# Performance work log

Measured on AMD Instinct MI355X. Metric: run time of the kernel, lower is better.

Reference implementation:

```python
import jax, jax.numpy as jnp
import numpy as np

N_HEAD = 4
GROUPS = 32
EPS = 1e-5


def group_norm(x, scale, bias):
    B, C, H, W = x.shape
    xg = x.reshape(B, GROUPS, C // GROUPS, H, W)
    mu = xg.mean(axis=(2, 3, 4), keepdims=True)
    var = xg.var(axis=(2, 3, 4), keepdims=True)
    xg = (xg - mu) * jax.lax.rsqrt(var + EPS)
    x = xg.reshape(B, C, H, W)
    return x * scale[None, :, None, None] + bias[None, :, None, None]


def setup_inputs() -> dict:
    key = jax.random.key(0)
    k0, k1, k2 = jax.random.split(key, 3)
    B, C, H, W = 2, 64, 64, 64
    x = jax.random.normal(k0, (B, C, H, W), dtype=jnp.float32)
    gn_scale = jnp.ones((C,), dtype=jnp.float32)
    gn_bias = jnp.zeros((C,), dtype=jnp.float32)
    w_qkv = jax.random.normal(k1, (3 * C, C), dtype=jnp.float32) * 0.05  # 1x1 conv, no bias
    w_out = jax.random.normal(k2, (C, C), dtype=jnp.float32) * 0.05     # 1x1 conv
    b_out = jnp.zeros((C,), dtype=jnp.float32)
    return {"x": x, "gn_scale": gn_scale, "gn_bias": gn_bias,
            "w_qkv": w_qkv, "w_out": w_out, "b_out": b_out}


def reference(x, gn_scale, gn_bias, w_qkv, w_out, b_out):
    B, C, H, W = x.shape
    head_dim = C // N_HEAD
    norm = group_norm(x, gn_scale, gn_bias)
    # 1x1 conv == channel matmul
    qkv = jnp.einsum('oc,bchw->bohw', w_qkv, norm)
    qkv = qkv.reshape(B, N_HEAD, head_dim * 3, H, W)
    q, k, v = jnp.split(qkv, 3, axis=2)  # each [B, n, head_dim, H, W]
    # full spatial attention scores, scaled by sqrt(channel) as in source
    attn = jnp.einsum('bnchw,bncyx->bnhwyx', q, k) / jnp.sqrt(jnp.float32(C))
    attn = jax.nn.softmax(attn.reshape(B, N_HEAD, H, W, H * W), axis=-1)
    attn = attn.reshape(B, N_HEAD, H, W, H, W)
    out = jnp.einsum('bnhwyx,bncyx->bnchw', attn, v).reshape(B, C, H, W)
    out = jnp.einsum('oc,bchw->bohw', w_out, out) + b_out[None, :, None, None]
    return out + x
```

## Files before the change

kernel.cpp:

```cpp
#include <hip/hip_runtime.h>
#include <hip/hip_bf16.h>

typedef __attribute__((ext_vector_type(8))) short short8;
typedef __attribute__((ext_vector_type(4))) float f32x4;
typedef __attribute__((ext_vector_type(16))) float f32x16;
typedef __attribute__((ext_vector_type(4))) unsigned int uint4v;
typedef __attribute__((ext_vector_type(4))) unsigned short ushort4v;

#define DEV static __device__ __forceinline__

DEV unsigned short f2bf(float f){
  unsigned u = __float_as_uint(f);
  u += 0x7fffu + ((u >> 16) & 1u);
  return (unsigned short)(u >> 16);
}

DEV float bf2f(unsigned short h){
  unsigned u = ((unsigned)h) << 16;
  float f;
  __builtin_memcpy(&f, &u, 4);
  return f;
}

DEV unsigned pack2bf(float a, float b){
  __hip_bfloat162 h = __float22bfloat162_rn(make_float2(a, b));
  unsigned u;
  __builtin_memcpy(&u, &h, 4);
  return u;
}

#define QSCALE 0.180336880111f
#define NSPLIT 8
#define NT 8

__global__ __launch_bounds__(256) void gn_partial_k(const float* __restrict__ x,
                                                    float* __restrict__ gp){
  int blk = blockIdx.x;
  float4 v = ((const float4*)(x + (size_t)blk*1024))[threadIdx.x];
  float s = v.x+v.y+v.z+v.w;
  float q = v.x*v.x+v.y*v.y+v.z*v.z+v.w*v.w;
  #pragma unroll
  for (int off = 1; off < 64; off <<= 1){
    s += __shfl_xor(s, off);
    q += __shfl_xor(q, off);
  }
  __shared__ float red[8];
  int w = threadIdx.x >> 6;
  if ((threadIdx.x & 63) == 0){ red[w*2] = s; red[w*2+1] = q; }
  __syncthreads();
  if (threadIdx.x == 0){
    gp[blk*2+0] = red[0]+red[2]+red[4]+red[6];
    gp[blk*2+1] = red[1]+red[3]+red[5]+red[7];
  }
}

__global__ __launch_bounds__(256) void qkv_k(const float* __restrict__ x,
    const float* __restrict__ gp, const float* __restrict__ gsc,
    const float* __restrict__ gbi, const float* __restrict__ wq,
    unsigned short* __restrict__ q, unsigned short* __restrict__ k,
    unsigned short* __restrict__ vt){
  int b  = blockIdx.x >> 8;
  int s0 = (blockIdx.x & 255) * 16;
  __shared__ float W[192][68];
  __shared__ float A[16][68];
  __shared__ float MS[32][2];
  int t = threadIdx.x;
  for (int i = t; i < 3072; i += 256){
    int o = i >> 4, c4 = (i & 15) * 4;
    *(float4*)&W[o][c4] = ((const float4*)wq)[i];
  }
  if (t < 32){
    float s = 0.f, ss = 0.f;
    #pragma unroll
    for (int i = 0; i < 8; ++i){
      const float* pp = gp + ((b*32 + t)*8 + i)*2;
      s += pp[0]; ss += pp[1];
    }
    float mean = s * (1.f/8192.f);
    MS[t][0] = mean;
    MS[t][1] = rsqrtf(ss * (1.f/8192.f) - mean*mean + 1e-5f);
  }
  __syncthreads();
  {
    int c  = t >> 2;
    int s4 = (t & 3) * 4;
    const float* px = x + ((size_t)b*64 + c)*4096 + s0 + s4;
    float4 v0 = *(const float4*)px;
    float sc = gsc[c] * MS[c>>1][1];
    float bi = gbi[c] - MS[c>>1][0] * sc;
    A[s4+0][c]=v0.x*sc+bi; A[s4+1][c]=v0.y*sc+bi;
    A[s4+2][c]=v0.z*sc+bi; A[s4+3][c]=v0.w*sc+bi;
  }
  __syncthreads();
  int sl = t >> 4, grp = t & 15;
  float acc[12];
  #pragma unroll
  for (int j = 0; j < 12; ++j) acc[j] = 0.f;
  for (int c4 = 0; c4 < 16; ++c4){
    float4 a = *(const float4*)&A[sl][c4*4];
    #pragma unroll
    for (int j = 0; j < 12; ++j){
      float4 wv = *(const float4*)&W[grp + j*16][c4*4];
      acc[j] = fmaf(a.x, wv.x, fmaf(a.y, wv.y, fmaf(a.z, wv.z, fmaf(a.w, wv.w, acc[j]))));
    }
  }
  int s = s0 + sl;
  int slp = (sl & 0x3) | (((sl >> 2) & 1) << 3) | (((sl >> 3) & 1) << 2);
  #pragma unroll
  for (int j = 0; j < 12; ++j){
    int o = grp + j*16;
    int n = o / 48, r = o % 48;
    float val = acc[j];
    if (r < 16){
      q[(((size_t)b*4 + n)*4096 + s)*16 + r] = f2bf(val * QSCALE);
    } else if (r < 32){
      k[(((size_t)b*4 + n)*4096 + s)*16 + r - 16] = f2bf(val);
    } else {
      vt[((size_t)(b*4 + n)*16 + (r - 32))*4096 + s0 + slp] = f2bf(val);
    }
  }
}

__global__ __launch_bounds__(256, 4) void attn_k(const unsigned short* __restrict__ qb,
    const unsigned short* __restrict__ kb, const unsigned short* __restrict__ vt,
    unsigned short* __restrict__ part, float* __restrict__ lsums){
  int blk = blockIdx.x;
  int bn = blk & 7;
  int sp = (blk >> 3) & (NSPLIT - 1);
  int qg = blk >> 6;
  int t = threadIdx.x, w = t >> 6, l = t & 63;
  int lq = l & 31, hi = l >> 5;

  __shared__ unsigned short Klds[8192];

  {
    const unsigned short* ksrc = kb + ((size_t)bn*4096 + sp*512)*16;
    #pragma unroll
    for (int p = 0; p < 4; ++p){
      int G = p*256 + t;
      *(short8*)&Klds[G*8] = *(const short8*)(ksrc + (size_t)G*8);
    }
  }

  int qrow = qg*128 + w*32;
  short8 qf = *(const short8*)(qb + ((size_t)bn*4096 + qrow)*16 + (size_t)lq*16 + hi*8);

  const unsigned short* vaddr = vt + ((size_t)bn*16 + (lq & 15))*4096 + sp*512 + hi*8;
  bool vld = (lq < 16);

  short8 vsel;
  {
    unsigned short c = (lq == 16) ? (unsigned short)0x3F80 : (unsigned short)0;
    #pragma unroll
    for (int r = 0; r < 8; ++r) vsel[r] = (short)c;
  }

  f32x16 O0, O1, zero;
  #pragma unroll
  for (int r = 0; r < 16; ++r){ O0[r] = 0.f; O1[r] = 0.f; zero[r] = 0.f; }

  __syncthreads();

  auto packP = [&](const f32x16& pc, int h8) -> short8 {
    uint4v pw;
    pw[0] = pack2bf(pc[h8+0], pc[h8+1]);
    pw[1] = pack2bf(pc[h8+2], pc[h8+3]);
    pw[2] = pack2bf(pc[h8+4], pc[h8+5]);
    pw[3] = pack2bf(pc[h8+6], pc[h8+7]);
    return __builtin_bit_cast(short8, pw);
  };

  short8 kf0 = *(const short8*)&Klds[(size_t)lq*16 + hi*8];
  short8 kf1 = *(const short8*)&Klds[(size_t)(32 + lq)*16 + hi*8];
  f32x16 sA = __builtin_amdgcn_mfma_f32_32x32x16_bf16(kf0, qf, zero, 0, 0, 0);
  f32x16 sB = __builtin_amdgcn_mfma_f32_32x32x16_bf16(kf1, qf, zero, 0, 0, 0);
  kf0 = *(const short8*)&Klds[(size_t)(64 + lq)*16 + hi*8];
  kf1 = *(const short8*)&Klds[(size_t)(96 + lq)*16 + hi*8];
  short8 v0 = vsel, v1 = vsel, v2 = vsel, v3 = vsel;
  if (vld){
    v0 = *(const short8*)(vaddr);
    v1 = *(const short8*)(vaddr + 16);
    v2 = *(const short8*)(vaddr + 32);
    v3 = *(const short8*)(vaddr + 48);
  }
  #pragma unroll
  for (int r = 0; r < 16; ++r) sA[r] = __builtin_amdgcn_exp2f(sA[r]);
  #pragma unroll
  for (int r = 0; r < 16; ++r) sB[r] = __builtin_amdgcn_exp2f(sB[r]);
  short8 paA0 = packP(sA, 0), paA1 = packP(sA, 8);
  short8 paB0 = packP(sB, 0), paB1 = packP(sB, 8);

  #pragma unroll 1
  for (int kt = 0; kt < NT-1; ++kt){
    __builtin_amdgcn_s_setprio(1);
    f32x16 nA = __builtin_amdgcn_mfma_f32_32x32x16_bf16(kf0, qf, zero, 0, 0, 0);
    f32x16 nB = __builtin_amdgcn_mfma_f32_32x32x16_bf16(kf1, qf, zero, 0, 0, 0);
    O0 = __builtin_amdgcn_mfma_f32_32x32x16_bf16(paA0, v0, O0, 0, 0, 0);
    O1 = __builtin_amdgcn_mfma_f32_32x32x16_bf16(paA1, v1, O1, 0, 0, 0);
    O0 = __builtin_amdgcn_mfma_f32_32x32x16_bf16(paB0, v2, O0, 0, 0, 0);
    O1 = __builtin_amdgcn_mfma_f32_32x32x16_bf16(paB1, v3, O1, 0, 0, 0);
    __builtin_amdgcn_s_setprio(0);
    if (kt + 2 < NT){
      kf0 = *(const short8*)&Klds[(size_t)((kt+2)*64 + lq)*16 + hi*8];
      kf1 = *(const short8*)&Klds[(size_t)((kt+2)*64 + 32 + lq)*16 + hi*8];
    }
    v0 = vsel; v1 = vsel; v2 = vsel; v3 = vsel;
    if (vld){
      const unsigned short* va = vaddr + (size_t)(kt+1)*64;
      v0 = *(const short8*)(va);
      v1 = *(const short8*)(va + 16);
      v2 = *(const short8*)(va + 32);
      v3 = *(const short8*)(va + 48);
    }
    #pragma unroll
    for (int r = 0; r < 16; ++r) nA[r] = __builtin_amdgcn_exp2f(nA[r]);
    #pragma unroll
    for (int r = 0; r < 16; ++r) nB[r] = __builtin_amdgcn_exp2f(nB[r]);
    paA0 = packP(nA, 0); paA1 = packP(nA, 8);
    paB0 = packP(nB, 0); paB1 = packP(nB, 8);
  }

  __builtin_amdgcn_s_setprio(1);
  O0 = __builtin_amdgcn_mfma_f32_32x32x16_bf16(paA0, v0, O0, 0, 0, 0);
  O1 = __builtin_amdgcn_mfma_f32_32x32x16_bf16(paA1, v1, O1, 0, 0, 0);
  O0 = __builtin_amdgcn_mfma_f32_32x32x16_bf16(paB0, v2, O0, 0, 0, 0);
  O1 = __builtin_amdgcn_mfma_f32_32x32x16_bf16(paB1, v3, O1, 0, 0, 0);
  __builtin_amdgcn_s_setprio(0);
  #pragma unroll
  for (int r = 0; r < 16; ++r) O0[r] += O1[r];

  unsigned short* Op = part + (((size_t)sp*8 + bn)*4096 + qrow)*16;
  size_t lbase = ((size_t)sp*8 + bn)*4096 + qrow;
  #pragma unroll
  for (int r = 0; r < 16; ++r){
    int qr = (r&3) + 8*(r>>2) + 4*hi;
    if (lq < 16) __builtin_nontemporal_store(f2bf(O0[r]), &Op[(size_t)qr*16 + lq]);
  }
  if (lq == 16){
    #pragma unroll
    for (int r = 0; r < 16; ++r){
      int qr = (r&3) + 8*(r>>2) + 4*hi;
      __builtin_nontemporal_store(O0[r], &lsums[lbase + qr]);
    }
  }
}

__global__ __launch_bounds__(256) void oproj_k(const unsigned short* __restrict__ part,
    const float* __restrict__ lsums, const float* __restrict__ wo,
    const float* __restrict__ bo, const float* __restrict__ x,
    float* __restrict__ out){
  int b  = blockIdx.x >> 8;
  int s0 = (blockIdx.x & 255) * 16;
  __shared__ float W[64][68];
  __shared__ float A[16][68];
  int t = threadIdx.x;
  for (int i = t; i < 1024; i += 256){
    int o = i >> 4, c4 = (i & 15) * 4;
    *(float4*)&W[o][c4] = ((const float4*)wo)[i];
  }
  {
    int sl = t & 15;
    int u  = t >> 4;
    int n = u >> 2, d4 = (u & 3) * 4;
    size_t row = ((size_t)b*4 + n)*4096 + s0 + sl;
    float L = 0.f;
    #pragma unroll
    for (int sp = 0; sp < NSPLIT; ++sp)
      L += __builtin_nontemporal_load(&lsums[(size_t)sp*32768 + row]);
    f32x4 acc = {0.f,0.f,0.f,0.f};
    #pragma unroll
    for (int sp = 0; sp < NSPLIT; ++sp){
      ushort4v u0 = *(const ushort4v*)(part + ((size_t)sp*32768 + row)*16 + d4);
      acc[0] += bf2f(u0[0]); acc[1] += bf2f(u0[1]);
      acc[2] += bf2f(u0[2]); acc[3] += bf2f(u0[3]);
    }
    float inv = 1.f / L;
    A[sl][n*16+d4+0] = acc[0]*inv; A[sl][n*16+d4+1] = acc[1]*inv;
    A[sl][n*16+d4+2] = acc[2]*inv; A[sl][n*16+d4+3] = acc[3]*inv;
  }
  __syncthreads();
  int sl = t & 15, grp = t >> 4;
  float acc[4] = {0.f,0.f,0.f,0.f};
  for (int c4 = 0; c4 < 16; ++c4){
    float4 a = *(const float4*)&A[sl][c4*4];
    #pragma unroll
    for (int j = 0; j < 4; ++j){
      float4 wv = *(const float4*)&W[grp + j*16][c4*4];
      acc[j] = fmaf(a.x, wv.x, fmaf(a.y, wv.y, fmaf(a.z, wv.z, fmaf(a.w, wv.w, acc[j]))));
    }
  }
  int s = s0 + sl;
  #pragma unroll
  for (int j = 0; j < 4; ++j){
    int o = grp + j*16;
    size_t idx = ((size_t)b*64 + o)*4096 + s;
    out[idx] = acc[j] + bo[o] + x[idx];
  }
}

extern "C" void kernel_launch(void* const* d_in, const int* in_sizes, int n_in,
                              void* d_out, int out_size, void* d_ws, size_t ws_size,
                              hipStream_t stream){
  const float* x   = (const float*)d_in[0];
  const float* gsc = (const float*)d_in[1];
  const float* gbi = (const float*)d_in[2];
  const float* wq  = (const float*)d_in[3];
  const float* wo  = (const float*)d_in[4];
  const float* bo  = (const float*)d_in[5];
  float* out = (float*)d_out;

  char* ws = (char*)d_ws;
  float* gp           = (float*)ws;
  unsigned short* q   = (unsigned short*)(ws + 8192);
  unsigned short* k   = (unsigned short*)(ws + 8192 + 1048576);
  unsigned short* vt  = (unsigned short*)(ws + 8192 + 2097152);
  unsigned short* part= (unsigned short*)(ws + 8192 + 3145728);
  float* lsums        = (float*)(ws + 8192 + 3145728 + 8388608);

  gn_partial_k<<<512,  256, 0, stream>>>(x, gp);
  qkv_k       <<<512,  256, 0, stream>>>(x, gp, gsc, gbi, wq, q, k, vt);
  attn_k      <<<2048, 256, 0, stream>>>(q, k, vt, part, lsums);
  oproj_k     <<<512,  256, 0, stream>>>(part, lsums, wo, bo, x, out);
}
```

Measured before the change: 55.60 us.

## Pad K tile in LDS, store ones-row in V, fully unroll attention loop

```diff
diff --git a/kernel.cpp b/kernel.cpp
--- a/kernel.cpp
+++ b/kernel.cpp
@@ -32,6 +32,7 @@
 #define QSCALE 0.180336880111f
 #define NSPLIT 8
 #define NT 8
+#define KSTRIDE 24
 
 __global__ __launch_bounds__(256) void gn_partial_k(const float* __restrict__ x,
                                                     float* __restrict__ gp){
@@ -80,6 +81,10 @@
     MS[t][0] = mean;
     MS[t][1] = rsqrtf(ss * (1.f/8192.f) - mean*mean + 1e-5f);
   }
+  if (t < 64){
+    int n = t >> 4, si = t & 15;
+    vt[((size_t)(b*4 + n)*32 + 16)*4096 + s0 + si] = (unsigned short)0x3F80;
+  }
   __syncthreads();
   {
     int c  = t >> 2;
@@ -116,7 +121,7 @@
     } else if (r < 32){
       k[(((size_t)b*4 + n)*4096 + s)*16 + r - 16] = f2bf(val);
     } else {
-      vt[((size_t)(b*4 + n)*16 + (r - 32))*4096 + s0 + slp] = f2bf(val);
+      vt[((size_t)(b*4 + n)*32 + (r - 32))*4096 + s0 + slp] = f2bf(val);
     }
   }
 }
@@ -131,29 +136,23 @@
   int t = threadIdx.x, w = t >> 6, l = t & 63;
   int lq = l & 31, hi = l >> 5;
 
-  __shared__ unsigned short Klds[8192];
+  __shared__ unsigned short Klds[512 * KSTRIDE];
 
   {
     const unsigned short* ksrc = kb + ((size_t)bn*4096 + sp*512)*16;
     #pragma unroll
     for (int p = 0; p < 4; ++p){
-      int G = p*256 + t;
-      *(short8*)&Klds[G*8] = *(const short8*)(ksrc + (size_t)G*8);
+      int g = p*256 + t;
+      int r = g >> 1, h = g & 1;
+      *(short8*)&Klds[r*KSTRIDE + h*8] = *(const short8*)(ksrc + (size_t)g*8);
     }
   }
 
   int qrow = qg*128 + w*32;
   short8 qf = *(const short8*)(qb + ((size_t)bn*4096 + qrow)*16 + (size_t)lq*16 + hi*8);
 
-  const unsigned short* vaddr = vt + ((size_t)bn*16 + (lq & 15))*4096 + sp*512 + hi*8;
-  bool vld = (lq < 16);
-
-  short8 vsel;
-  {
-    unsigned short c = (lq == 16) ? (unsigned short)0x3F80 : (unsigned short)0;
-    #pragma unroll
-    for (int r = 0; r < 8; ++r) vsel[r] = (short)c;
-  }
+  int vrow = (lq < 16) ? lq : 16;
+  const unsigned short* vaddr = vt + ((size_t)bn*32 + vrow)*4096 + sp*512 + hi*8;
 
   f32x16 O0, O1, zero;
   #pragma unroll
@@ -170,62 +169,37 @@
     return __builtin_bit_cast(short8, pw);
   };
 
-  short8 kf0 = *(const short8*)&Klds[(size_t)lq*16 + hi*8];
-  short8 kf1 = *(const short8*)&Klds[(size_t)(32 + lq)*16 + hi*8];
-  f32x16 sA = __builtin_amdgcn_mfma_f32_32x32x16_bf16(kf0, qf, zero, 0, 0, 0);
-  f32x16 sB = __builtin_amdgcn_mfma_f32_32x32x16_bf16(kf1, qf, zero, 0, 0, 0);
-  kf0 = *(const short8*)&Klds[(size_t)(64 + lq)*16 + hi*8];
-  kf1 = *(const short8*)&Klds[(size_t)(96 + lq)*16 + hi*8];
-  short8 v0 = vsel, v1 = vsel, v2 = vsel, v3 = vsel;
-  if (vld){
-    v0 = *(const short8*)(vaddr);
-    v1 = *(const short8*)(vaddr + 16);
-    v2 = *(const short8*)(vaddr + 32);
-    v3 = *(const short8*)(vaddr + 48);
-  }
-  #pragma unroll
-  for (int r = 0; r < 16; ++r) sA[r] = __builtin_amdgcn_exp2f(sA[r]);
-  #pragma unroll
-  for (int r = 0; r < 16; ++r) sB[r] = __builtin_amdgcn_exp2f(sB[r]);
-  short8 paA0 = packP(sA, 0), paA1 = packP(sA, 8);
-  short8 paB0 = packP(sB, 0), paB1 = packP(sB, 8);
-
-  #pragma unroll 1
-  for (int kt = 0; kt < NT-1; ++kt){
+  #pragma unroll
+  for (int kt = 0; kt < NT; ++kt){
+    const unsigned short* va = vaddr + kt*64;
+    short8 v0 = *(const short8*)(va);
+    short8 v1 = *(const short8*)(va + 16);
+    short8 v2 = *(const short8*)(va + 32);
+    short8 v3 = *(const short8*)(va + 48);
+    short8 kf0 = *(const short8*)&Klds[(kt*64 + lq)*KSTRIDE + hi*8];
+    short8 kf1 = *(const short8*)&Klds[(kt*64 + 32 + lq)*KSTRIDE + hi*8];
+
     __builtin_amdgcn_s_setprio(1);
-    f32x16 nA = __builtin_amdgcn_mfma_f32_32x32x16_bf16(kf0, qf, zero, 0, 0, 0);
-    f32x16 nB = __builtin_amdgcn_mfma_f32_32x32x16_bf16(kf1, qf, zero, 0, 0, 0);
+    f32x16 sA = __builtin_amdgcn_mfma_f32_32x32x16_bf16(kf0, qf, zero, 0, 0, 0);
+    f32x16 sB = __builtin_amdgcn_mfma_f32_32x32x16_bf16(kf1, qf, zero, 0, 0, 0);
+    __builtin_amdgcn_s_setprio(0);
+
+    #pragma unroll
+    for (int r = 0; r < 16; ++r) sA[r] = __builtin_amdgcn_exp2f(sA[r]);
+    #pragma unroll
+    for (int r = 0; r < 16; ++r) sB[r] = __builtin_amdgcn_exp2f(sB[r]);
+
+    short8 paA0 = packP(sA, 0), paA1 = packP(sA, 8);
+    short8 paB0 = packP(sB, 0), paB1 = packP(sB, 8);
+
+    __builtin_amdgcn_s_setprio(1);
     O0 = __builtin_amdgcn_mfma_f32_32x32x16_bf16(paA0, v0, O0, 0, 0, 0);
     O1 = __builtin_amdgcn_mfma_f32_32x32x16_bf16(paA1, v1, O1, 0, 0, 0);
     O0 = __builtin_amdgcn_mfma_f32_32x32x16_bf16(paB0, v2, O0, 0, 0, 0);
     O1 = __builtin_amdgcn_mfma_f32_32x32x16_bf16(paB1, v3, O1, 0, 0, 0);
     __builtin_amdgcn_s_setprio(0);
-    if (kt + 2 < NT){
-      kf0 = *(const short8*)&Klds[(size_t)((kt+2)*64 + lq)*16 + hi*8];
-      kf1 = *(const short8*)&Klds[(size_t)((kt+2)*64 + 32 + lq)*16 + hi*8];
-    }
-    v0 = vsel; v1 = vsel; v2 = vsel; v3 = vsel;
-    if (vld){
-      const unsigned short* va = vaddr + (size_t)(kt+1)*64;
-      v0 = *(const short8*)(va);
-      v1 = *(const short8*)(va + 16);
-      v2 = *(const short8*)(va + 32);
-      v3 = *(const short8*)(va + 48);
-    }
-    #pragma unroll
-    for (int r = 0; r < 16; ++r) nA[r] = __builtin_amdgcn_exp2f(nA[r]);
-    #pragma unroll
-    for (int r = 0; r < 16; ++r) nB[r] = __builtin_amdgcn_exp2f(nB[r]);
-    paA0 = packP(nA, 0); paA1 = packP(nA, 8);
-    paB0 = packP(nB, 0); paB1 = packP(nB, 8);
-  }
-
-  __builtin_amdgcn_s_setprio(1);
-  O0 = __builtin_amdgcn_mfma_f32_32x32x16_bf16(paA0, v0, O0, 0, 0, 0);
-  O1 = __builtin_amdgcn_mfma_f32_32x32x16_bf16(paA1, v1, O1, 0, 0, 0);
-  O0 = __builtin_amdgcn_mfma_f32_32x32x16_bf16(paB0, v2, O0, 0, 0, 0);
-  O1 = __builtin_amdgcn_mfma_f32_32x32x16_bf16(paB1, v3, O1, 0, 0, 0);
-  __builtin_amdgcn_s_setprio(0);
+  }
+
   #pragma unroll
   for (int r = 0; r < 16; ++r) O0[r] += O1[r];
 
@@ -314,8 +288,8 @@
   unsigned short* q   = (unsigned short*)(ws + 8192);
   unsigned short* k   = (unsigned short*)(ws + 8192 + 1048576);
   unsigned short* vt  = (unsigned short*)(ws + 8192 + 2097152);
-  unsigned short* part= (unsigned short*)(ws + 8192 + 3145728);
-  float* lsums        = (float*)(ws + 8192 + 3145728 + 8388608);
+  unsigned short* part= (unsigned short*)(ws + 8192 + 4194304);
+  float* lsums        = (float*)(ws + 8192 + 4194304 + 8388608);
 
   gn_partial_k<<<512,  256, 0, stream>>>(x, gp);
   qkv_k       <<<512,  256, 0, stream>>>(x, gp, gsc, gbi, wq, q, k, vt);
```

After: 54.93 us. No clear change (-1.2%).
